# Kernel tuning notes

Measured on AMD Instinct MI355X. Metric: run time of the kernel, lower is better.

## Reference

```python
import jax, jax.numpy as jnp
import numpy as np

N = 256
B = 4

def setup_inputs() -> dict:
    key = jax.random.key(0)
    k1, k2 = jax.random.split(key)
    volume = jax.random.normal(k1, (N, N, N), dtype=jnp.float32)
    quaternions = jax.random.normal(k2, (B, 4), dtype=jnp.float32)
    return {"volume": volume, "quaternions": quaternions}


def _quat_to_R(q):
    # normalize then build 3x3 rotation matrix (differentiable)
    q = q / jnp.linalg.norm(q)
    qw, qx, qy, qz = q[0], q[1], q[2], q[3]
    return jnp.stack([
        jnp.stack([1 - 2 * (qy**2 + qz**2), 2 * (qx*qy - qz*qw), 2 * (qx*qz + qy*qw)]),
        jnp.stack([2 * (qx*qy + qz*qw), 1 - 2 * (qx**2 + qz**2), 2 * (qy*qz - qx*qw)]),
        jnp.stack([2 * (qx*qz - qy*qw), 2 * (qy*qz + qx*qw), 1 - 2 * (qx**2 + qy**2)]),
    ])


def _trilinear(volume, gx, gy, gz):
    """grid_sample(align_corners=True) equivalent.
    volume: (N,N,N) indexed as (D,H,W); gx/gy/gz: pixel-space coords,
    gx indexes W (last axis), gy indexes H, gz indexes D."""
    n = volume.shape[0]
    fx0, fy0, fz0 = jnp.floor(gx), jnp.floor(gy), jnp.floor(gz)
    tx, ty, tz = gx - fx0, gy - fy0, gz - fz0
    x0 = jnp.clip(fx0.astype(jnp.int32), 0, n - 1)
    y0 = jnp.clip(fy0.astype(jnp.int32), 0, n - 1)
    z0 = jnp.clip(fz0.astype(jnp.int32), 0, n - 1)
    x1 = jnp.clip(x0 + 1, 0, n - 1)
    y1 = jnp.clip(y0 + 1, 0, n - 1)
    z1 = jnp.clip(z0 + 1, 0, n - 1)
    v = lambda zi, yi, xi: volume[zi, yi, xi]
    c00 = v(z0, y0, x0) * (1 - tx) + v(z0, y0, x1) * tx
    c01 = v(z0, y1, x0) * (1 - tx) + v(z0, y1, x1) * tx
    c10 = v(z1, y0, x0) * (1 - tx) + v(z1, y0, x1) * tx
    c11 = v(z1, y1, x0) * (1 - tx) + v(z1, y1, x1) * tx
    c0 = c00 * (1 - ty) + c01 * ty
    c1 = c10 * (1 - ty) + c11 * ty
    return c0 * (1 - tz) + c1 * tz


def reference(volume, quaternions):
    n = volume.shape[0]
    half = n / 2.0
    x = jnp.arange(n, dtype=jnp.float32) - half
    xx, yy, zz = jnp.meshgrid(x, x, x, indexing='ij')
    grid = jnp.stack([xx, yy, zz], axis=-1).reshape(-1, 3)  # (N^3, 3)

    def one(q):
        R = _quat_to_R(q)
        rg = jnp.clip((grid @ R.T) / half, -1.0, 1.0)  # (N^3, 3) in [-1,1]
        pix = (rg + 1.0) * 0.5 * (n - 1)  # align_corners=True mapping
        # grid_sample convention: channel 0 -> W (x), 1 -> H (y), 2 -> D (z)
        vals = _trilinear(volume, pix[:, 0], pix[:, 1], pix[:, 2])
        rot = vals.reshape(n, n, n)
        return rot.sum(axis=2)  # project along dim=2

    return jax.vmap(one)(quaternions)
```

## Files before the change

kernel.cpp:

```cpp
#include <hip/hip_runtime.h>
#include <hip/hip_fp16.h>


#define NN 256

typedef unsigned uv4 __attribute__((ext_vector_type(4)));


__device__ __forceinline__ unsigned pack2h(float lo, float hi) {
    __half2 h = __floats2half2_rn(lo, hi);
    return *reinterpret_cast<unsigned*>(&h);
}

__device__ __forceinline__ float2 unpack2h(unsigned u) {
    __half2 h = *reinterpret_cast<__half2*>(&u);
    return __half22float2(h);
}


__global__ __launch_bounds__(256) void pack4hb_kernel(
    const float* __restrict__ vol, uint2* __restrict__ v4)
{
    const int t = blockIdx.x * 256 + threadIdx.x;
    const int x4 = (t & 63) << 2;
    const int zy = t >> 6;
    const int y = zy & 255;
    const int y1 = min(y + 1, NN - 1);
    const int z = zy >> 8;

    const float* r0 = vol + ((z << 16) | (y  << 8));
    const float* r1 = vol + ((z << 16) | (y1 << 8));
    const float4 p0 = *reinterpret_cast<const float4*>(r0 + x4);
    const float4 p1 = *reinterpret_cast<const float4*>(r1 + x4);
    const float n0 = (x4 == 252) ? p0.w : r0[x4 + 4];
    const float n1 = (x4 == 252) ? p1.w : r1[x4 + 4];

    uv4 lo, hi;
    lo.x = pack2h(p0.x, p0.y);  lo.y = pack2h(p1.x, p1.y);
    lo.z = pack2h(p0.y, p0.z);  lo.w = pack2h(p1.y, p1.z);
    hi.x = pack2h(p0.z, p0.w);  hi.y = pack2h(p1.z, p1.w);
    hi.z = pack2h(p0.w, n0);    hi.w = pack2h(p1.w, n1);

    const int bidx = ((z >> 3) << 19) | ((y >> 3) << 14) | ((x4 >> 3) << 9)
                   | ((z & 7) << 6)  | ((y & 7) << 3)   | (x4 & 7);
    uv4* dst = reinterpret_cast<uv4*>(v4 + bidx);
    dst[0] = lo;
    dst[1] = hi;
}


struct RayCtx {
    float bPx, bPy, bPz;
    float dPx, dPy, dPz;
};

__device__ __forceinline__ RayCtx make_ray(const float* __restrict__ quats,
                                           int b, int i, int j)
{
    const float q0 = quats[b * 4 + 0];
    const float q1 = quats[b * 4 + 1];
    const float q2 = quats[b * 4 + 2];
    const float q3 = quats[b * 4 + 3];
    const float nrm = sqrtf(q0 * q0 + q1 * q1 + q2 * q2 + q3 * q3);
    const float qw = q0 / nrm, qx = q1 / nrm, qy = q2 / nrm, qz = q3 / nrm;

    const float r00 = 1.0f - 2.0f * (qy * qy + qz * qz);
    const float r01 = 2.0f * (qx * qy - qz * qw);
    const float r02 = 2.0f * (qx * qz + qy * qw);
    const float r10 = 2.0f * (qx * qy + qz * qw);
    const float r11 = 1.0f - 2.0f * (qx * qx + qz * qz);
    const float r12 = 2.0f * (qy * qz - qx * qw);
    const float r20 = 2.0f * (qx * qz - qy * qw);
    const float r21 = 2.0f * (qy * qz + qx * qw);
    const float r22 = 1.0f - 2.0f * (qx * qx + qy * qy);

    const float gi = (float)i - 128.0f;
    const float gj = (float)j - 128.0f;

    const float bx = gi * r00 + gj * r01;
    const float by = gi * r10 + gj * r11;
    const float bz = gi * r20 + gj * r21;

    const float K = 127.5f / 128.0f;
    RayCtx c;
    c.dPx = r02 * K;  c.dPy = r12 * K;  c.dPz = r22 * K;
    c.bPx = bx * K + 127.5f;
    c.bPy = by * K + 127.5f;
    c.bPz = bz * K + 127.5f;
    return c;
}


__global__ __launch_bounds__(256) void rotproj4hb_kernel(
    const uint2* __restrict__ v4,
    const float* __restrict__ quats,
    float* __restrict__ out)
{
    const int tid = threadIdx.x;
    const int w = tid >> 6;
    const int l = tid & 63;
    const int di = l & 3;
    const int dj = (l >> 2) & 3;
    const int dk = l >> 4;

    const int b = blockIdx.z;
    const int i = blockIdx.y * 8 + ((w & 1) << 2) + di;
    const int j = blockIdx.x * 8 + ((w >> 1) << 2) + dj;

    const RayCtx c = make_ray(quats, b, i, j);

    float acc = 0.0f;
    float kf = (float)dk - 128.0f;

#pragma unroll 8
    for (int t = 0; t < 64; ++t) {
        float px = fminf(fmaxf(fmaf(kf, c.dPx, c.bPx), 0.0f), 255.0f);
        float py = fminf(fmaxf(fmaf(kf, c.dPy, c.bPy), 0.0f), 255.0f);
        float pz = fminf(fmaxf(fmaf(kf, c.dPz, c.bPz), 0.0f), 255.0f);
        kf += 4.0f;

        const int x0 = (int)px;
        const int y0 = (int)py;
        const int z0 = (int)pz;
        const float tfx = __builtin_amdgcn_fractf(px);
        const float tfy = __builtin_amdgcn_fractf(py);
        const float tfz = __builtin_amdgcn_fractf(pz);
        const int z1 = z0 + (z0 < NN - 1 ? 1 : 0);

        const int yx = ((y0 >> 3) << 14) | ((x0 >> 3) << 9)
                     | ((y0 & 7) << 3)  | (x0 & 7);
        const int za = ((z0 >> 3) << 19) | ((z0 & 7) << 6);
        const int zd = ((z1 >> 3) << 19) | ((z1 & 7) << 6);

        const uint2 A = v4[yx | za];
        const uint2 D = v4[yx | zd];

        const float2 a0 = unpack2h(A.x);
        const float2 a1 = unpack2h(A.y);
        const float2 d0 = unpack2h(D.x);
        const float2 d1 = unpack2h(D.y);

        const float ux = 1.0f - tfx, uy = 1.0f - tfy, uz = 1.0f - tfz;
        const float c00 = a0.x * ux + a0.y * tfx;
        const float c01 = a1.x * ux + a1.y * tfx;
        const float c10 = d0.x * ux + d0.y * tfx;
        const float c11 = d1.x * ux + d1.y * tfx;
        const float c0 = c00 * uy + c01 * tfy;
        const float c1 = c10 * uy + c11 * tfy;
        acc += c0 * uz + c1 * tfz;
    }

    acc += __shfl_xor(acc, 16, 64);
    acc += __shfl_xor(acc, 32, 64);
    if (dk == 0) {
        out[(b << 16) | (i << 8) | j] = acc;
    }
}


__global__ __launch_bounds__(256) void rotproj_direct_kernel(
    const float* __restrict__ vol,
    const float* __restrict__ quats,
    float* __restrict__ out)
{
    const int tx = threadIdx.x & 7;
    const int ty = (threadIdx.x >> 3) & 7;
    const int tz = threadIdx.x >> 6;
    const int b = blockIdx.z;
    const int i = blockIdx.y * 8 + ty;
    const int j = blockIdx.x * 8 + tx;

    const RayCtx c = make_ray(quats, b, i, j);

    float acc = 0.0f;
    float kf = (float)(tz * 64) - 128.0f;
#pragma unroll 4
    for (int kk = 0; kk < 64; ++kk) {
        float px = fminf(fmaxf(fmaf(kf, c.dPx, c.bPx), 0.0f), 255.0f);
        float py = fminf(fmaxf(fmaf(kf, c.dPy, c.bPy), 0.0f), 255.0f);
        float pz = fminf(fmaxf(fmaf(kf, c.dPz, c.bPz), 0.0f), 255.0f);
        kf += 1.0f;

        const int x0 = (int)px, y0 = (int)py, z0 = (int)pz;
        const float tfx = __builtin_amdgcn_fractf(px);
        const float tfy = __builtin_amdgcn_fractf(py);
        const float tfz = __builtin_amdgcn_fractf(pz);
        const int x1 = min(x0 + 1, NN - 1);
        const int y1 = min(y0 + 1, NN - 1);
        const int z1 = min(z0 + 1, NN - 1);

        const float* row00 = vol + ((z0 << 16) | (y0 << 8));
        const float* row01 = vol + ((z0 << 16) | (y1 << 8));
        const float* row10 = vol + ((z1 << 16) | (y0 << 8));
        const float* row11 = vol + ((z1 << 16) | (y1 << 8));

        const float v000 = row00[x0], v001 = row00[x1];
        const float v010 = row01[x0], v011 = row01[x1];
        const float v100 = row10[x0], v101 = row10[x1];
        const float v110 = row11[x0], v111 = row11[x1];

        const float ux = 1.0f - tfx, uy = 1.0f - tfy, uz = 1.0f - tfz;
        const float c00 = v000 * ux + v001 * tfx;
        const float c01 = v010 * ux + v011 * tfx;
        const float c10 = v100 * ux + v101 * tfx;
        const float c11 = v110 * ux + v111 * tfx;
        const float c0 = c00 * uy + c01 * tfy;
        const float c1 = c10 * uy + c11 * tfy;
        acc += c0 * uz + c1 * tfz;
    }

    __shared__ float sm[4][8][8];
    sm[tz][ty][tx] = acc;
    __syncthreads();
    if (tz == 0) {
        out[(b << 16) | (i << 8) | j] =
            sm[0][ty][tx] + sm[1][ty][tx] + sm[2][ty][tx] + sm[3][ty][tx];
    }
}


extern "C" void kernel_launch(void* const* d_in, const int* in_sizes, int n_in,
                              void* d_out, int out_size, void* d_ws, size_t ws_size,
                              hipStream_t stream) {
    const float* vol = (const float*)d_in[0];
    const float* quats = (const float*)d_in[1];
    float* out = (float*)d_out;

    const int B = in_sizes[1] / 4;
    const size_t nvox = (size_t)NN * NN * NN;
    const size_t need = nvox * sizeof(uint2);

    dim3 grid(NN / 8, NN / 8, B);
    dim3 block(256, 1, 1);

    if (ws_size >= need) {
        uint2* v4 = (uint2*)d_ws;
        const int pack_blocks = (int)(nvox / 4 / 256);
        hipLaunchKernelGGL(pack4hb_kernel, dim3(pack_blocks), dim3(256), 0, stream,
                           vol, v4);
        hipLaunchKernelGGL(rotproj4hb_kernel, grid, block, 0, stream,
                           v4, quats, out);
    } else {
        hipLaunchKernelGGL(rotproj_direct_kernel, grid, block, 0, stream,
                           vol, quats, out);
    }
}
```

Baseline: 247.7 us.

## Stage pack via shared-memory brick tiles and swizzle projection block order across XCDs

The packing kernel now loads 9 volume rows per z-slice into LDS and writes each 8x8x8 brick contiguously, so global stores are coalesced. Before, each thread wrote two scattered 16-byte vectors and reloaded neighbouring values from global memory. The projection kernel switches to a 1D grid with a block-index remap, so consecutive tiles are spread across the 8 XCDs, which may change how L2 locality is shared. The risks are LDS sync overhead in the pack and a remap that assumes a 32x32 tile grid per batch.

```diff
diff --git a/kernel.cpp b/kernel.cpp
--- a/kernel.cpp
+++ b/kernel.cpp
@@ -3,8 +3,6 @@
 
 
 #define NN 256
-
-typedef unsigned uv4 __attribute__((ext_vector_type(4)));
 
 
 __device__ __forceinline__ unsigned pack2h(float lo, float hi) {
@@ -18,34 +16,47 @@
 }
 
 
-__global__ __launch_bounds__(256) void pack4hb_kernel(
+__global__ __launch_bounds__(256) void packbrick_kernel(
     const float* __restrict__ vol, uint2* __restrict__ v4)
 {
-    const int t = blockIdx.x * 256 + threadIdx.x;
-    const int x4 = (t & 63) << 2;
-    const int zy = t >> 6;
-    const int y = zy & 255;
-    const int y1 = min(y + 1, NN - 1);
-    const int z = zy >> 8;
-
-    const float* r0 = vol + ((z << 16) | (y  << 8));
-    const float* r1 = vol + ((z << 16) | (y1 << 8));
-    const float4 p0 = *reinterpret_cast<const float4*>(r0 + x4);
-    const float4 p1 = *reinterpret_cast<const float4*>(r1 + x4);
-    const float n0 = (x4 == 252) ? p0.w : r0[x4 + 4];
-    const float n1 = (x4 == 252) ? p1.w : r1[x4 + 4];
-
-    uv4 lo, hi;
-    lo.x = pack2h(p0.x, p0.y);  lo.y = pack2h(p1.x, p1.y);
-    lo.z = pack2h(p0.y, p0.z);  lo.w = pack2h(p1.y, p1.z);
-    hi.x = pack2h(p0.z, p0.w);  hi.y = pack2h(p1.z, p1.w);
-    hi.z = pack2h(p0.w, n0);    hi.w = pack2h(p1.w, n1);
-
-    const int bidx = ((z >> 3) << 19) | ((y >> 3) << 14) | ((x4 >> 3) << 9)
-                   | ((z & 7) << 6)  | ((y & 7) << 3)   | (x4 & 7);
-    uv4* dst = reinterpret_cast<uv4*>(v4 + bidx);
-    dst[0] = lo;
-    dst[1] = hi;
+    __shared__ float rows[9][260];
+
+    const int zb = blockIdx.x >> 5;
+    const int yb = blockIdx.x & 31;
+    const int tid = threadIdx.x;
+    const int w = tid >> 6;
+    const int l = tid & 63;
+    const int y7 = l >> 3;
+    const int x7 = l & 7;
+
+    for (int z7 = 0; z7 < 8; ++z7) {
+        const int z = (zb << 3) | z7;
+
+        __syncthreads();
+        for (int r = tid; r < 576; r += 256) {
+            const int row = r >> 6;
+            const int xg = (r & 63) << 2;
+            const int y = min((yb << 3) + row, NN - 1);
+            const float4 v = *reinterpret_cast<const float4*>(
+                vol + ((z << 16) | (y << 8) | xg));
+            *reinterpret_cast<float4*>(&rows[row][xg]) = v;
+        }
+        __syncthreads();
+
+        const int base = (zb << 19) | (yb << 14) | (z7 << 6);
+#pragma unroll
+        for (int xi = 0; xi < 8; ++xi) {
+            const int xb = (xi << 2) | w;
+            const int x = (xb << 3) | x7;
+            const int xp = min(x + 1, NN - 1);
+            const float v00 = rows[y7][x],     v01 = rows[y7][xp];
+            const float v10 = rows[y7 + 1][x], v11 = rows[y7 + 1][xp];
+            uint2 g;
+            g.x = pack2h(v00, v01);
+            g.y = pack2h(v10, v11);
+            v4[base | (xb << 9) | l] = g;
+        }
+    }
 }
 
 
@@ -96,6 +107,12 @@
     const float* __restrict__ quats,
     float* __restrict__ out)
 {
+    const int q8 = gridDim.x >> 3;
+    const int wg = (blockIdx.x & 7) * q8 + (blockIdx.x >> 3);
+    const int b = wg >> 10;
+    const int by = (wg >> 5) & 31;
+    const int bx = wg & 31;
+
     const int tid = threadIdx.x;
     const int w = tid >> 6;
     const int l = tid & 63;
@@ -103,9 +120,8 @@
     const int dj = (l >> 2) & 3;
     const int dk = l >> 4;
 
-    const int b = blockIdx.z;
-    const int i = blockIdx.y * 8 + ((w & 1) << 2) + di;
-    const int j = blockIdx.x * 8 + ((w >> 1) << 2) + dj;
+    const int i = (by << 3) + ((w & 1) << 2) + di;
+    const int j = (bx << 3) + ((w >> 1) << 2) + dj;
 
     const RayCtx c = make_ray(quats, b, i, j);
 
@@ -230,18 +246,15 @@
     const size_t nvox = (size_t)NN * NN * NN;
     const size_t need = nvox * sizeof(uint2);
 
-    dim3 grid(NN / 8, NN / 8, B);
-    dim3 block(256, 1, 1);
-
     if (ws_size >= need) {
         uint2* v4 = (uint2*)d_ws;
-        const int pack_blocks = (int)(nvox / 4 / 256);
-        hipLaunchKernelGGL(pack4hb_kernel, dim3(pack_blocks), dim3(256), 0, stream,
+        hipLaunchKernelGGL(packbrick_kernel, dim3(1024), dim3(256), 0, stream,
                            vol, v4);
-        hipLaunchKernelGGL(rotproj4hb_kernel, grid, block, 0, stream,
-                           v4, quats, out);
+        hipLaunchKernelGGL(rotproj4hb_kernel, dim3(1024 * B), dim3(256), 0,
+                           stream, v4, quats, out);
     } else {
-        hipLaunchKernelGGL(rotproj_direct_kernel, grid, block, 0, stream,
+        dim3 grid(NN / 8, NN / 8, B);
+        hipLaunchKernelGGL(rotproj_direct_kernel, grid, dim3(256), 0, stream,
                            vol, quats, out);
     }
 }
```

New measurement: 265.7 us. +7.3%, slower.
